# Kernel optimization log

Hardware: AMD Instinct MI355X
Metric: run time of the kernel (lower is better)

Reference implementation:

```python
import jax, jax.numpy as jnp
import numpy as np

NUM_HEADS = 12

def setup_inputs() -> dict:
    key = jax.random.key(0)
    ks = jax.random.split(key, 7)
    B, Np, C = 512, 255, 768
    w_std = C ** -0.5  # keep pre-softmax logits well-scaled
    return {
        "x": jax.random.normal(ks[0], (B, 1, C), jnp.float32),
        "prompts": jax.random.normal(ks[1], (B, Np, C), jnp.float32),
        "wq": jax.random.normal(ks[2], (C, C), jnp.float32) * w_std,
        "bq": jnp.zeros((C,), jnp.float32),
        "wk": jax.random.normal(ks[3], (C, C), jnp.float32) * w_std,
        "bk": jnp.zeros((C,), jnp.float32),
        "wv": jax.random.normal(ks[4], (C, C), jnp.float32) * w_std,
        "bv": jnp.zeros((C,), jnp.float32),
        "wp": jax.random.normal(ks[5], (C, C), jnp.float32) * w_std,
        "bp": jnp.zeros((C,), jnp.float32),
    }


def reference(x, prompts, wq, bq, wk, bk, wv, bv, wp, bp):
    # x: [B,1,C], prompts: [B,Np,C]. Default config: more_prompts=1,
    # cross_attn_wo_x=False, return_all_tokens=False, residual=True, no dropout.
    B, N, C = x.shape
    H = NUM_HEADS
    hd = C // H
    scale = hd ** -0.5  # 0.125
    L = prompts.shape[1] + N  # k/v length = N_prompts + 1

    xp = jnp.concatenate([x, prompts], axis=1)          # [B,L,C]
    q = (x @ wq + bq).reshape(B, N, H, hd) * scale       # [B,1,H,hd]
    k = (xp @ wk + bk).reshape(B, L, H, hd)              # [B,L,H,hd]
    v = (xp @ wv + bv).reshape(B, L, H, hd)              # [B,L,H,hd]

    raw_attn = jnp.einsum('bqhd,blhd->bhql', q, k)       # [B,H,1,L] pre-softmax
    attn = jax.nn.softmax(raw_attn, axis=-1) * scale     # unusual post-softmax rescale
    ctx = jnp.einsum('bhql,blhd->bqhd', attn, v).reshape(B, N, C)

    x_cls = ctx @ wp + bp + x                            # proj + residual
    return x_cls, raw_attn
```

## Files before the change

kernel.cpp:

```cpp
#include <hip/hip_runtime.h>
#include <hip/hip_bf16.h>


#define SCALE 0.125f

template<bool BT>
__global__ __launch_bounds__(256) void gemm_k(
    const float* __restrict__ A, int lda, int aZ,
    const float* __restrict__ B, int ldb, int bZ,
    const float* __restrict__ bias, int biasZ, float bscale,
    const float* __restrict__ res,
    float* __restrict__ C, int ldc, int cZ,
    int K, float mul)
{
    __shared__ float As[16][68];
    __shared__ float Bs[16][68];
    const int tid = threadIdx.x;
    const int n0 = blockIdx.x * 64;
    const int m0 = blockIdx.y * 64;
    const int z  = blockIdx.z;
    const float* Ab = A + (size_t)z * aZ;

    float acc[4][4];
#pragma unroll
    for (int i = 0; i < 4; ++i)
#pragma unroll
        for (int j = 0; j < 4; ++j) acc[i][j] = 0.f;

    const int tx = tid & 15;
    const int ty = tid >> 4;

    for (int k0 = 0; k0 < K; k0 += 16) {
        __syncthreads();
        {
            const int i = tid >> 2, kq = tid & 3;
            float4 v = *(const float4*)&Ab[(size_t)(m0 + i) * lda + k0 + 4*kq];
            As[4*kq+0][i] = v.x; As[4*kq+1][i] = v.y;
            As[4*kq+2][i] = v.z; As[4*kq+3][i] = v.w;
        }
        if (!BT) {
            const int kk = tid >> 4, n4 = tid & 15;
            float4 v = *(const float4*)&B[(size_t)(k0 + kk) * ldb + (size_t)z*bZ + n0 + 4*n4];
            *(float4*)&Bs[kk][4*n4] = v;
        } else {
            const int nn = tid >> 2, kq = tid & 3;
            float4 v = *(const float4*)&B[(size_t)(n0 + nn) * ldb + (size_t)z*bZ + k0 + 4*kq];
            Bs[4*kq+0][nn] = v.x; Bs[4*kq+1][nn] = v.y;
            Bs[4*kq+2][nn] = v.z; Bs[4*kq+3][nn] = v.w;
        }
        __syncthreads();
#pragma unroll
        for (int kk = 0; kk < 16; ++kk) {
            float4 a4 = *(const float4*)&As[kk][4*ty];
            float4 b4 = *(const float4*)&Bs[kk][4*tx];
            float av[4] = {a4.x, a4.y, a4.z, a4.w};
            float bv[4] = {b4.x, b4.y, b4.z, b4.w};
#pragma unroll
            for (int i = 0; i < 4; ++i)
#pragma unroll
                for (int j = 0; j < 4; ++j) acc[i][j] += av[i] * bv[j];
        }
    }

    float* Cb = C + (size_t)z * cZ;
    float bv4[4] = {0.f, 0.f, 0.f, 0.f};
    if (bias) {
        float4 bb = *(const float4*)&bias[(size_t)z*biasZ + n0 + 4*tx];
        bv4[0] = bscale*bb.x; bv4[1] = bscale*bb.y; bv4[2] = bscale*bb.z; bv4[3] = bscale*bb.w;
    }
#pragma unroll
    for (int i = 0; i < 4; ++i) {
        const int m = m0 + 4*ty + i;
        float v[4];
#pragma unroll
        for (int j = 0; j < 4; ++j) v[j] = mul * acc[i][j] + bv4[j];
        if (res) {
            float4 rv = *(const float4*)&res[(size_t)m * 768 + n0 + 4*tx];
            v[0] += rv.x; v[1] += rv.y; v[2] += rv.z; v[3] += rv.w;
        }
        float4 out = {v[0], v[1], v[2], v[3]};
        *(float4*)&Cb[(size_t)m * ldc + n0 + 4*tx] = out;
    }
}

__global__ __launch_bounds__(256) void qbk_k(
    const float* __restrict__ q, const float* __restrict__ bk,
    float* __restrict__ qbk)
{
    const int task = blockIdx.x * 4 + (threadIdx.x >> 6);
    const int ln = threadIdx.x & 63;
    const int b = task / 12, h = task % 12;
    float v = q[(size_t)b * 768 + h * 64 + ln] * bk[h * 64 + ln];
#pragma unroll
    for (int off = 32; off > 0; off >>= 1) v += __shfl_xor(v, off);
    if (ln == 0) qbk[task] = v;
}

__global__ __launch_bounds__(256, 2) void attn_fused_k(
    const float* __restrict__ x, const float* __restrict__ prompts,
    const float* __restrict__ qk_in, const float* __restrict__ qbk,
    float* __restrict__ s_out, float* __restrict__ raw_attn)
{
    __shared__ float xs[16 * 772];
    __shared__ float p_lds[12 * 256];
    const int b = blockIdx.x;
    const int tid = threadIdx.x;
    const int wid = tid >> 6, ln = tid & 63;

    float qkr[3][12];
    float qb[3];
#pragma unroll
    for (int h3 = 0; h3 < 3; ++h3) {
        const int h = 3 * wid + h3;
        const float* base = qk_in + ((size_t)(b * 12 + h)) * 768 + 4 * ln;
#pragma unroll
        for (int qc = 0; qc < 3; ++qc) {
            float4 v = *(const float4*)(base + qc * 256);
            qkr[h3][qc*4+0] = v.x; qkr[h3][qc*4+1] = v.y;
            qkr[h3][qc*4+2] = v.z; qkr[h3][qc*4+3] = v.w;
        }
        qb[h3] = qbk[b * 12 + h];
    }

    float acc[3][12];
#pragma unroll
    for (int h3 = 0; h3 < 3; ++h3)
#pragma unroll
        for (int j = 0; j < 12; ++j) acc[h3][j] = 0.f;
    float dsum[3] = {0.f, 0.f, 0.f};

    for (int t = 0; t < 16; ++t) {
        __syncthreads();
#pragma unroll
        for (int i = 0; i < 12; ++i) {
            const int f = tid + 256 * i;
            const int row = f / 192, c4 = f % 192;
            const int l = t * 16 + row;
            const float* src = (l == 0)
                ? (x + (size_t)b * 768 + 4 * c4)
                : (prompts + ((size_t)b * 255 + (l - 1)) * 768 + 4 * c4);
            float4 v = *(const float4*)src;
            *(float4*)&xs[row * 772 + 4 * c4] = v;
        }
        __syncthreads();

        for (int r = 0; r < 16; ++r) {
            const int l = t * 16 + r;
            float xv[12];
#pragma unroll
            for (int qc = 0; qc < 3; ++qc) {
                float4 v = *(const float4*)&xs[r * 772 + qc * 256 + 4 * ln];
                xv[qc*4+0] = v.x; xv[qc*4+1] = v.y;
                xv[qc*4+2] = v.z; xv[qc*4+3] = v.w;
            }
            float lg[3];
#pragma unroll
            for (int h3 = 0; h3 < 3; ++h3) {
                float p = 0.f;
#pragma unroll
                for (int j = 0; j < 12; ++j) p += xv[j] * qkr[h3][j];
#pragma unroll
                for (int off = 32; off > 0; off >>= 1) p += __shfl_xor(p, off);
                lg[h3] = p + qb[h3];
            }
            if (ln == 0) {
                p_lds[(3*wid + 0) * 256 + l] = lg[0];
                p_lds[(3*wid + 1) * 256 + l] = lg[1];
                p_lds[(3*wid + 2) * 256 + l] = lg[2];
            }
#pragma unroll
            for (int h3 = 0; h3 < 3; ++h3) {
                const float e = exp2f(lg[h3] * 1.44269504088896f);
                dsum[h3] += e;
#pragma unroll
                for (int j = 0; j < 12; ++j) acc[h3][j] += e * xv[j];
            }
        }
    }

#pragma unroll
    for (int h3 = 0; h3 < 3; ++h3) {
        const float inv = SCALE / dsum[h3];
        const int h = 3 * wid + h3;
        float* base = s_out + ((size_t)(b * 12 + h)) * 768 + 4 * ln;
#pragma unroll
        for (int qc = 0; qc < 3; ++qc) {
            float4 v = {acc[h3][qc*4+0] * inv, acc[h3][qc*4+1] * inv,
                        acc[h3][qc*4+2] * inv, acc[h3][qc*4+3] * inv};
            *(float4*)(base + qc * 256) = v;
        }
    }

    __syncthreads();
#pragma unroll
    for (int i = 0; i < 12; ++i)
        raw_attn[(size_t)b * 3072 + i * 256 + tid] = p_lds[i * 256 + tid];
}

extern "C" void kernel_launch(void* const* d_in, const int* in_sizes, int n_in,
                              void* d_out, int out_size, void* d_ws, size_t ws_size,
                              hipStream_t stream) {
    const float* x       = (const float*)d_in[0];
    const float* prompts = (const float*)d_in[1];
    const float* wq      = (const float*)d_in[2];
    const float* bq      = (const float*)d_in[3];
    const float* wk      = (const float*)d_in[4];
    const float* bk      = (const float*)d_in[5];
    const float* wv      = (const float*)d_in[6];
    const float* bv      = (const float*)d_in[7];
    const float* wp      = (const float*)d_in[8];
    const float* bp      = (const float*)d_in[9];

    float* out_x    = (float*)d_out;
    float* out_attn = out_x + 512 * 768;

    float* q_ws   = (float*)d_ws;
    float* qk_ws  = q_ws + 512 * 768;
    float* qbk_ws = qk_ws + 512 * 12 * 768;
    float* ctx_ws = q_ws;

    hipLaunchKernelGGL((gemm_k<false>), dim3(12, 8, 1), dim3(256), 0, stream,
        x, 768, 0,  wq, 768, 0,  bq, 0, SCALE,  nullptr,
        q_ws, 768, 0,  768, SCALE);

    hipLaunchKernelGGL(qbk_k, dim3(1536), dim3(256), 0, stream,
        q_ws, bk, qbk_ws);

    hipLaunchKernelGGL((gemm_k<true>), dim3(12, 8, 12), dim3(256), 0, stream,
        q_ws, 768, 64,  wk, 768, 64,  nullptr, 0, 0.f,  nullptr,
        qk_ws, 9216, 768,  64, 1.0f);

    hipLaunchKernelGGL(attn_fused_k, dim3(512), dim3(256), 0, stream,
        x, prompts, qk_ws, qbk_ws, qk_ws, out_attn);

    hipLaunchKernelGGL((gemm_k<false>), dim3(1, 8, 12), dim3(256), 0, stream,
        qk_ws, 9216, 768,  wv, 768, 64,  bv, 64, SCALE,  nullptr,
        ctx_ws, 768, 64,  768, 1.0f);

    hipLaunchKernelGGL((gemm_k<false>), dim3(12, 8, 1), dim3(256), 0, stream,
        ctx_ws, 768, 0,  wp, 768, 0,  bp, 0, 1.0f,  x,
        out_x, 768, 0,  768, 1.0f);
}
```

Baseline: 777.2 us.

## Split-K the small GEMMs and batch attention logit reductions through LDS

The q, ctx and output projection GEMMs now split their K dimension four ways, writing partial sums to a workspace. A new reduce kernel sums the partials and applies bias, scale and the residual, so far more blocks run on what were underfilled grids. Inside the fused attention kernel, logits for four rows are computed together and reduced through LDS with short shuffles, replacing a full 64-lane shuffle reduction per row and head, and the exponentials are shared via a small LDS buffer. This adds three extra launches and extra workspace traffic, and relies on LDS writes and reads within a wavefront without an explicit barrier.

```diff
diff --git a/kernel.cpp b/kernel.cpp
--- a/kernel.cpp
+++ b/kernel.cpp
@@ -10,8 +10,8 @@
     const float* __restrict__ B, int ldb, int bZ,
     const float* __restrict__ bias, int biasZ, float bscale,
     const float* __restrict__ res,
-    float* __restrict__ C, int ldc, int cZ,
-    int K, float mul)
+    float* __restrict__ C, int ldc, int cZ, long pStride,
+    int K, int kParts, float mul)
 {
     __shared__ float As[16][68];
     __shared__ float Bs[16][68];
@@ -19,7 +19,11 @@
     const int n0 = blockIdx.x * 64;
     const int m0 = blockIdx.y * 64;
     const int z  = blockIdx.z;
-    const float* Ab = A + (size_t)z * aZ;
+    const int zH = z / kParts;
+    const int zK = z % kParts;
+    const int kLen = K / kParts;
+    const int kOff = zK * kLen;
+    const float* Ab = A + (size_t)zH * aZ;
 
     float acc[4][4];
 #pragma unroll
@@ -30,21 +34,21 @@
     const int tx = tid & 15;
     const int ty = tid >> 4;
 
-    for (int k0 = 0; k0 < K; k0 += 16) {
+    for (int k0 = 0; k0 < kLen; k0 += 16) {
         __syncthreads();
         {
             const int i = tid >> 2, kq = tid & 3;
-            float4 v = *(const float4*)&Ab[(size_t)(m0 + i) * lda + k0 + 4*kq];
+            float4 v = *(const float4*)&Ab[(size_t)(m0 + i) * lda + kOff + k0 + 4*kq];
             As[4*kq+0][i] = v.x; As[4*kq+1][i] = v.y;
             As[4*kq+2][i] = v.z; As[4*kq+3][i] = v.w;
         }
         if (!BT) {
             const int kk = tid >> 4, n4 = tid & 15;
-            float4 v = *(const float4*)&B[(size_t)(k0 + kk) * ldb + (size_t)z*bZ + n0 + 4*n4];
+            float4 v = *(const float4*)&B[(size_t)(kOff + k0 + kk) * ldb + (size_t)zH*bZ + n0 + 4*n4];
             *(float4*)&Bs[kk][4*n4] = v;
         } else {
             const int nn = tid >> 2, kq = tid & 3;
-            float4 v = *(const float4*)&B[(size_t)(n0 + nn) * ldb + (size_t)z*bZ + k0 + 4*kq];
+            float4 v = *(const float4*)&B[(size_t)(n0 + nn) * ldb + (size_t)zH*bZ + kOff + k0 + 4*kq];
             Bs[4*kq+0][nn] = v.x; Bs[4*kq+1][nn] = v.y;
             Bs[4*kq+2][nn] = v.z; Bs[4*kq+3][nn] = v.w;
         }
@@ -62,10 +66,10 @@
         }
     }
 
-    float* Cb = C + (size_t)z * cZ;
+    float* Cb = C + (size_t)zH * cZ + (size_t)zK * pStride;
     float bv4[4] = {0.f, 0.f, 0.f, 0.f};
     if (bias) {
-        float4 bb = *(const float4*)&bias[(size_t)z*biasZ + n0 + 4*tx];
+        float4 bb = *(const float4*)&bias[(size_t)zH*biasZ + n0 + 4*tx];
         bv4[0] = bscale*bb.x; bv4[1] = bscale*bb.y; bv4[2] = bscale*bb.z; bv4[3] = bscale*bb.w;
     }
 #pragma unroll
@@ -81,6 +85,31 @@
         float4 out = {v[0], v[1], v[2], v[3]};
         *(float4*)&Cb[(size_t)m * ldc + n0 + 4*tx] = out;
     }
+}
+
+__global__ __launch_bounds__(256) void reduce_k(
+    const float* __restrict__ part, long pStride, int S,
+    const float* __restrict__ bias, float bscale,
+    const float* __restrict__ res,
+    float* __restrict__ out, float mul)
+{
+    const int f4 = blockIdx.x * 256 + threadIdx.x;
+    const int idx = f4 * 4;
+    const int n = idx % 768;
+    float4 a = *(const float4*)&part[idx];
+#pragma unroll 4
+    for (int s = 1; s < S; ++s) {
+        float4 p = *(const float4*)&part[(size_t)s * pStride + idx];
+        a.x += p.x; a.y += p.y; a.z += p.z; a.w += p.w;
+    }
+    float4 bb = *(const float4*)&bias[n];
+    float4 v = {mul*a.x + bscale*bb.x, mul*a.y + bscale*bb.y,
+                mul*a.z + bscale*bb.z, mul*a.w + bscale*bb.w};
+    if (res) {
+        float4 rv = *(const float4*)&res[idx];
+        v.x += rv.x; v.y += rv.y; v.z += rv.z; v.w += rv.w;
+    }
+    *(float4*)&out[idx] = v;
 }
 
 __global__ __launch_bounds__(256) void qbk_k(
@@ -103,9 +132,12 @@
 {
     __shared__ float xs[16 * 772];
     __shared__ float p_lds[12 * 256];
+    __shared__ float red[4][12][68];
+    __shared__ float ebuf[4][16];
     const int b = blockIdx.x;
     const int tid = threadIdx.x;
     const int wid = tid >> 6, ln = tid & 63;
+    const int pair = ln >> 2, seg = ln & 3;
 
     float qkr[3][12];
     float qb[3];
@@ -121,6 +153,7 @@
         }
         qb[h3] = qbk[b * 12 + h];
     }
+    const float qb_sel = (pair >= 8) ? qb[2] : ((pair >= 4) ? qb[1] : qb[0]);
 
     float acc[3][12];
 #pragma unroll
@@ -144,36 +177,69 @@
         }
         __syncthreads();
 
-        for (int r = 0; r < 16; ++r) {
-            const int l = t * 16 + r;
-            float xv[12];
-#pragma unroll
-            for (int qc = 0; qc < 3; ++qc) {
-                float4 v = *(const float4*)&xs[r * 772 + qc * 256 + 4 * ln];
-                xv[qc*4+0] = v.x; xv[qc*4+1] = v.y;
-                xv[qc*4+2] = v.z; xv[qc*4+3] = v.w;
-            }
-            float lg[3];
+        for (int g = 0; g < 4; ++g) {
+            const int l0 = t * 16 + 4 * g;
+            float xvb[4][12];
+            float pp[3][4];
+#pragma unroll
+            for (int r = 0; r < 4; ++r) {
+#pragma unroll
+                for (int qc = 0; qc < 3; ++qc) {
+                    float4 v = *(const float4*)&xs[(4*g + r) * 772 + qc * 256 + 4 * ln];
+                    xvb[r][qc*4+0] = v.x; xvb[r][qc*4+1] = v.y;
+                    xvb[r][qc*4+2] = v.z; xvb[r][qc*4+3] = v.w;
+                }
+#pragma unroll
+                for (int h3 = 0; h3 < 3; ++h3) {
+                    float p = 0.f;
+#pragma unroll
+                    for (int j = 0; j < 12; ++j) p += xvb[r][j] * qkr[h3][j];
+                    pp[h3][r] = p;
+                }
+            }
+#pragma unroll
+            for (int h3 = 0; h3 < 3; ++h3)
+#pragma unroll
+                for (int r = 0; r < 4; ++r)
+                    red[wid][h3*4 + r][ln] = pp[h3][r];
+
+            float tot = 0.f;
+            if (pair < 12) {
+                const float* rp = &red[wid][pair][16 * seg];
+                float4 s0 = *(const float4*)(rp + 0);
+                float4 s1 = *(const float4*)(rp + 4);
+                float4 s2 = *(const float4*)(rp + 8);
+                float4 s3 = *(const float4*)(rp + 12);
+                tot = ((s0.x+s0.y)+(s0.z+s0.w)) + ((s1.x+s1.y)+(s1.z+s1.w))
+                    + ((s2.x+s2.y)+(s2.z+s2.w)) + ((s3.x+s3.y)+(s3.z+s3.w));
+            }
+            tot += __shfl_xor(tot, 1);
+            tot += __shfl_xor(tot, 2);
+            tot += qb_sel;
+            if (pair < 12) {
+                if (seg == 0) {
+                    p_lds[(3*wid + (pair >> 2)) * 256 + l0 + (pair & 3)] = tot;
+                    ebuf[wid][pair] = exp2f(tot * 1.44269504088896f);
+                }
+            }
+            float ev[12];
+            {
+                float4 e0 = *(const float4*)&ebuf[wid][0];
+                float4 e1 = *(const float4*)&ebuf[wid][4];
+                float4 e2 = *(const float4*)&ebuf[wid][8];
+                ev[0]=e0.x; ev[1]=e0.y; ev[2]=e0.z; ev[3]=e0.w;
+                ev[4]=e1.x; ev[5]=e1.y; ev[6]=e1.z; ev[7]=e1.w;
+                ev[8]=e2.x; ev[9]=e2.y; ev[10]=e2.z; ev[11]=e2.w;
+            }
 #pragma unroll
             for (int h3 = 0; h3 < 3; ++h3) {
-                float p = 0.f;
-#pragma unroll
-                for (int j = 0; j < 12; ++j) p += xv[j] * qkr[h3][j];
-#pragma unroll
-                for (int off = 32; off > 0; off >>= 1) p += __shfl_xor(p, off);
-                lg[h3] = p + qb[h3];
-            }
-            if (ln == 0) {
-                p_lds[(3*wid + 0) * 256 + l] = lg[0];
-                p_lds[(3*wid + 1) * 256 + l] = lg[1];
-                p_lds[(3*wid + 2) * 256 + l] = lg[2];
-            }
-#pragma unroll
-            for (int h3 = 0; h3 < 3; ++h3) {
-                const float e = exp2f(lg[h3] * 1.44269504088896f);
-                dsum[h3] += e;
-#pragma unroll
-                for (int j = 0; j < 12; ++j) acc[h3][j] += e * xv[j];
+#pragma unroll
+                for (int r = 0; r < 4; ++r) {
+                    const float e = ev[h3*4 + r];
+                    dsum[h3] += e;
+#pragma unroll
+                    for (int j = 0; j < 12; ++j) acc[h3][j] += e * xvb[r][j];
+                }
             }
         }
     }
@@ -215,29 +281,38 @@
     float* out_attn = out_x + 512 * 768;
 
     float* q_ws   = (float*)d_ws;
-    float* qk_ws  = q_ws + 512 * 768;
-    float* qbk_ws = qk_ws + 512 * 12 * 768;
+    float* qk_ws  = q_ws + 393216;
+    float* qbk_ws = qk_ws + 4718592;
+    float* part   = qbk_ws + 8192;
     float* ctx_ws = q_ws;
 
-    hipLaunchKernelGGL((gemm_k<false>), dim3(12, 8, 1), dim3(256), 0, stream,
-        x, 768, 0,  wq, 768, 0,  bq, 0, SCALE,  nullptr,
-        q_ws, 768, 0,  768, SCALE);
+    const long PS = 393216;
+
+    hipLaunchKernelGGL((gemm_k<false>), dim3(12, 8, 4), dim3(256), 0, stream,
+        x, 768, 0,  wq, 768, 0,  nullptr, 0, 0.f,  nullptr,
+        part, 768, 0, PS,  768, 4, 1.0f);
+    hipLaunchKernelGGL(reduce_k, dim3(384), dim3(256), 0, stream,
+        part, PS, 4, bq, SCALE, nullptr, q_ws, SCALE);
 
     hipLaunchKernelGGL(qbk_k, dim3(1536), dim3(256), 0, stream,
         q_ws, bk, qbk_ws);
 
     hipLaunchKernelGGL((gemm_k<true>), dim3(12, 8, 12), dim3(256), 0, stream,
         q_ws, 768, 64,  wk, 768, 64,  nullptr, 0, 0.f,  nullptr,
-        qk_ws, 9216, 768,  64, 1.0f);
+        qk_ws, 9216, 768, 0,  64, 1, 1.0f);
 
     hipLaunchKernelGGL(attn_fused_k, dim3(512), dim3(256), 0, stream,
         x, prompts, qk_ws, qbk_ws, qk_ws, out_attn);
 
-    hipLaunchKernelGGL((gemm_k<false>), dim3(1, 8, 12), dim3(256), 0, stream,
-        qk_ws, 9216, 768,  wv, 768, 64,  bv, 64, SCALE,  nullptr,
-        ctx_ws, 768, 64,  768, 1.0f);
-
-    hipLaunchKernelGGL((gemm_k<false>), dim3(12, 8, 1), dim3(256), 0, stream,
-        ctx_ws, 768, 0,  wp, 768, 0,  bp, 0, 1.0f,  x,
-        out_x, 768, 0,  768, 1.0f);
-}
+    hipLaunchKernelGGL((gemm_k<false>), dim3(1, 8, 48), dim3(256), 0, stream,
+        qk_ws, 9216, 768,  wv, 768, 64,  nullptr, 0, 0.f,  nullptr,
+        part, 768, 64, PS,  768, 4, 1.0f);
+    hipLaunchKernelGGL(reduce_k, dim3(384), dim3(256), 0, stream,
+        part, PS, 4, bv, SCALE, nullptr, ctx_ws, 1.0f);
+
+    hipLaunchKernelGGL((gemm_k<false>), dim3(12, 8, 4), dim3(256), 0, stream,
+        ctx_ws, 768, 0,  wp, 768, 0,  nullptr, 0, 0.f,  nullptr,
+        part, 768, 0, PS,  768, 4, 1.0f);
+    hipLaunchKernelGGL(reduce_k, dim3(384), dim3(256), 0, stream,
+        part, PS, 4, bp, 1.0f, x, out_x, 1.0f);
+}
```

Result: slower. 1.030 ms (+32.5%).
